# Kernel optimization log

Measured on AMD Instinct MI355X. Metric: run time of the kernel, lower is better.

## Reference

```python
import jax, jax.numpy as jnp
import numpy as np

MARGIN = 1.0  # init kwarg margin=1; hard_mining=False path


def setup_inputs() -> dict:
    key = jax.random.key(0)
    k1, k2 = jax.random.split(key)
    inputs = jax.random.normal(k1, (4096, 128), dtype=jnp.float32)
    targets = jax.random.randint(k2, (4096,), 0, 64, dtype=jnp.int64)
    return {"inputs": inputs, "targets": targets}


def reference(inputs, targets):
    n = inputs.shape[0]
    # squared pairwise distances: ||xi||^2 + ||xj||^2 - 2 xi.xj, relu'd then sqrt
    sq = jnp.sum(inputs * inputs, axis=1)                      # [n]
    d2 = jnp.maximum(sq[:, None] + sq[None, :] - 2.0 * (inputs @ inputs.T), 0.0)
    nz = d2 > 0
    dist = jnp.where(nz, jnp.sqrt(jnp.where(nz, d2, 1.0)), 0.0)  # safe sqrt, [n,n]

    eye = jnp.eye(n, dtype=bool)
    same = targets[:, None] == targets[None, :]
    pos_mask = same & ~eye            # positive pairs, diag removed
    neg_mask = ~same                  # negative pairs

    # torch code gathers neg_dist[i].nonzero(): negatives with nonzero distance
    neg_valid = neg_mask & (dist != 0.0)
    row_neg = jnp.sum(jnp.where(neg_valid, jnp.exp(MARGIN - dist), 0.0), axis=1)  # [n]

    # loop runs over upper-triangular positive pairs (diag already excluded)
    idx = jnp.arange(n)
    triu_pos = pos_mask & (idx[:, None] < idx[None, :])
    J = jnp.log(row_neg[:, None] + row_neg[None, :]) + dist    # Jij_heat
    contrib = jnp.where(triu_pos, jax.nn.relu(J) ** 2, 0.0)

    len_p = jnp.sum(pos_mask).astype(inputs.dtype)             # count over FULL pos_mask
    return jnp.sum(contrib) / len_p
```

## Files before the change

### kernel.cpp

```cpp
#include <hip/hip_runtime.h>
#include <hip/hip_bf16.h>
#include <math.h>

typedef short short8 __attribute__((ext_vector_type(8)));
typedef float f32x4 __attribute__((ext_vector_type(4)));

#define NROW 4096
#define DIM  128
#define NCLS 64
#define MAXM 128
#define LCAP 256
#define NBT  64
#define NTILE 2080
#define PS   66

__device__ __forceinline__ unsigned short f2bf(float f) {
    unsigned u = __builtin_bit_cast(unsigned, f);
    unsigned r = (u + 0x7fffu + ((u >> 16) & 1u)) >> 16;
    return (unsigned short)r;
}

__device__ __forceinline__ short8 pack8(const float4& a, const float4& b) {
    short8 h;
    h[0] = (short)f2bf(a.x); h[1] = (short)f2bf(a.y);
    h[2] = (short)f2bf(a.z); h[3] = (short)f2bf(a.w);
    h[4] = (short)f2bf(b.x); h[5] = (short)f2bf(b.y);
    h[6] = (short)f2bf(b.z); h[7] = (short)f2bf(b.w);
    return h;
}

__global__ __launch_bounds__(256, 4) void rowneg_kernel(
        const float* __restrict__ X, const int* __restrict__ tgt,
        float* __restrict__ P, float* __restrict__ acc, unsigned* __restrict__ tick)
{
    const int t = threadIdx.x;
    const int w = t >> 6, l = t & 63, lr = l & 15, lg = l >> 4;

    const int k = blockIdx.x;
    int bi = (int)(64.5f - sqrtf(64.5f * 64.5f - 2.0f * (float)k));
    if (bi < 0) bi = 0; if (bi > NBT - 1) bi = NBT - 1;
    while (bi < NBT - 1 && ((bi + 1) * NBT - (((bi + 1) * bi) >> 1)) <= k) ++bi;
    while (bi > 0 && (bi * NBT - ((bi * (bi - 1)) >> 1)) > k) --bi;
    const int bj = bi + (k - (bi * NBT - ((bi * (bi - 1)) >> 1)));
    const int gib = bi * 64, gjb = bj * 64;

    __shared__ __align__(16) unsigned short tA[64 * 128];
    __shared__ __align__(16) unsigned short tB[64 * 128];
    __shared__ float s_sqi[64], s_sqj[64];
    __shared__ float s_cacc[4][64];
    __shared__ int   s_ti[64], s_tj[64];

    {
        const int row  = t >> 1;
        const int half = t & 1;
        const int grow = (row < 64) ? (gib + row) : (gjb + row - 64);
        const float4* src = reinterpret_cast<const float4*>(X + (size_t)grow * DIM + half * 64);
        float4 buf[16];
        #pragma unroll
        for (int q = 0; q < 16; ++q) buf[q] = src[q];
        float p = 0.0f;
        #pragma unroll
        for (int q = 0; q < 16; ++q)
            p += buf[q].x * buf[q].x + buf[q].y * buf[q].y + buf[q].z * buf[q].z + buf[q].w * buf[q].w;
        p += __shfl_xor(p, 1);
        unsigned short* dst = (row < 64) ? tA : tB;
        const int lrow = row & 63;
        #pragma unroll
        for (int q = 0; q < 8; ++q) {
            int c16 = half * 8 + q;
            *reinterpret_cast<short8*>(&dst[lrow * 128 + ((c16 ^ (lrow & 7)) * 8)]) =
                pack8(buf[2 * q], buf[2 * q + 1]);
        }
        if (half == 0) {
            if (row < 64) s_sqi[row] = p; else s_sqj[row - 64] = p;
        }
    }
    if (t < 64)       s_ti[t] = tgt[gib + t];
    else if (t < 128) s_tj[t - 64] = tgt[gjb + t - 64];
    else if (k == 0 && t < 131) {
        if (t == 128) acc[0] = 0.0f;
        if (t == 129) acc[1] = 0.0f;
        if (t == 130) tick[0] = 0u;
    }
    __syncthreads();

    const int arow = w * 16 + lr;
    f32x4 C[4] = {};
    #pragma unroll
    for (int ks = 0; ks < 4; ++ks) {
        int c = ks * 4 + lg;
        short8 a = *reinterpret_cast<const short8*>(&tA[arow * 128 + ((c ^ (arow & 7)) * 8)]);
        #pragma unroll
        for (int fj = 0; fj < 4; ++fj) {
            int brow = fj * 16 + lr;
            short8 bb = *reinterpret_cast<const short8*>(&tB[brow * 128 + ((c ^ (brow & 7)) * 8)]);
            C[fj] = __builtin_amdgcn_mfma_f32_16x16x32_bf16(a, bb, C[fj], 0, 0, 0);
        }
    }

    const int ibase = w * 16 + lg * 4;
    float sqi[4]; int ti[4];
    #pragma unroll
    for (int r = 0; r < 4; ++r) { sqi[r] = s_sqi[ibase + r]; ti[r] = s_ti[ibase + r]; }

    float racc[4] = {0.f, 0.f, 0.f, 0.f};
    float cacc[4] = {0.f, 0.f, 0.f, 0.f};
    #pragma unroll
    for (int fj = 0; fj < 4; ++fj) {
        int jl = fj * 16 + lr;
        float sqj = s_sqj[jl];
        int   tj  = s_tj[jl];
        int   gj  = gjb + jl;
        #pragma unroll
        for (int r = 0; r < 4; ++r) {
            int gi = gib + ibase + r;
            float d2 = fmaxf(sqi[r] + sqj - 2.0f * C[fj][r], 0.0f);
            float dist = __builtin_amdgcn_sqrtf(d2);
            float e = __expf(1.0f - dist);
            bool valid = (gi < gj) && (ti[r] != tj) && (d2 > 0.0f);
            e = valid ? e : 0.0f;
            racc[r] += e;
            cacc[fj] += e;
        }
    }

    #pragma unroll
    for (int r = 0; r < 4; ++r) {
        racc[r] += __shfl_xor(racc[r], 1);
        racc[r] += __shfl_xor(racc[r], 2);
        racc[r] += __shfl_xor(racc[r], 4);
        racc[r] += __shfl_xor(racc[r], 8);
    }
    if (lr == 0) {
        #pragma unroll
        for (int r = 0; r < 4; ++r)
            P[(size_t)(gib + ibase + r) * PS + (bj + 1)] = racc[r];
    }
    #pragma unroll
    for (int fj = 0; fj < 4; ++fj) {
        cacc[fj] += __shfl_xor(cacc[fj], 16);
        cacc[fj] += __shfl_xor(cacc[fj], 32);
    }
    if (lg == 0) {
        #pragma unroll
        for (int fj = 0; fj < 4; ++fj) s_cacc[w][fj * 16 + lr] = cacc[fj];
    }
    __syncthreads();
    if (t < 64) {
        float cs = s_cacc[0][t] + s_cacc[1][t] + s_cacc[2][t] + s_cacc[3][t];
        P[(size_t)(gjb + t) * PS + bi] = cs;
    }
}

__global__ __launch_bounds__(256) void loss_kernel(
        const float* __restrict__ X, const int* __restrict__ tgt,
        const float* __restrict__ P,
        float* __restrict__ acc, unsigned* __restrict__ tick, float* __restrict__ out)
{
    const int c = blockIdx.x >> 1;
    const int h = blockIdx.x & 1;

    __shared__ __align__(16) unsigned short tX[MAXM * DIM];
    __shared__ float sqg[MAXM], rng[MAXM];
    __shared__ int   s_idx[LCAP];
    __shared__ int   s_wsum[4];
    __shared__ float s_red[16];

    const int t = threadIdx.x;
    const int w = t >> 6, l = t & 63, lr = l & 15, lg = l >> 4;

    float csum = 0.0f, cpairs = 0.0f;
    int mtot, mm, nfj;

    {
        const int rbase = t * 16;
        int tv[16];
        {
            int4 a = *reinterpret_cast<const int4*>(tgt + rbase);
            int4 b = *reinterpret_cast<const int4*>(tgt + rbase + 4);
            int4 d = *reinterpret_cast<const int4*>(tgt + rbase + 8);
            int4 e = *reinterpret_cast<const int4*>(tgt + rbase + 12);
            tv[0]=a.x; tv[1]=a.y; tv[2]=a.z; tv[3]=a.w;
            tv[4]=b.x; tv[5]=b.y; tv[6]=b.z; tv[7]=b.w;
            tv[8]=d.x; tv[9]=d.y; tv[10]=d.z; tv[11]=d.w;
            tv[12]=e.x; tv[13]=e.y; tv[14]=e.z; tv[15]=e.w;
        }
        int cnt = 0;
        #pragma unroll
        for (int k2 = 0; k2 < 16; ++k2) cnt += (tv[k2] == c) ? 1 : 0;
        int sc = cnt;
        #pragma unroll
        for (int d2 = 1; d2 < 64; d2 <<= 1) {
            int u = __shfl_up(sc, d2);
            if (l >= d2) sc += u;
        }
        if (l == 63) s_wsum[w] = sc;
        __syncthreads();
        int woff = 0;
        if (w > 0) woff += s_wsum[0];
        if (w > 1) woff += s_wsum[1];
        if (w > 2) woff += s_wsum[2];
        int off = woff + sc - cnt;
        #pragma unroll
        for (int k2 = 0; k2 < 16; ++k2) {
            if (tv[k2] == c) { if (off < LCAP) s_idx[off] = rbase + k2; ++off; }
        }
        mtot = s_wsum[0] + s_wsum[1] + s_wsum[2] + s_wsum[3];
    }
    mm  = mtot < MAXM ? mtot : MAXM;
    nfj = (mm + 15) >> 4;
    __syncthreads();

    if (h == 1 && mm <= 64) goto tickout;

    if (t < MAXM) {
        float s2 = 0.0f;
        if (t < mm) {
            const float* pp = P + (size_t)s_idx[t] * PS;
            #pragma unroll 5
            for (int s = 0; s < 65; ++s) s2 += pp[s];
        }
        rng[t] = s2;
    }

    {
        const int row  = t >> 1;
        const int half = t & 1;
        if (row < mm) {
            const int ri = s_idx[row];
            const float4* src = reinterpret_cast<const float4*>(X + (size_t)ri * DIM + half * 64);
            float4 buf[16];
            #pragma unroll
            for (int q = 0; q < 16; ++q) buf[q] = src[q];
            float p = 0.0f;
            #pragma unroll
            for (int q = 0; q < 16; ++q)
                p += buf[q].x * buf[q].x + buf[q].y * buf[q].y + buf[q].z * buf[q].z + buf[q].w * buf[q].w;
            p += __shfl_xor(p, 1);
            #pragma unroll
            for (int q = 0; q < 8; ++q) {
                int c16 = half * 8 + q;
                *reinterpret_cast<short8*>(&tX[row * 128 + ((c16 ^ (row & 7)) * 8)]) =
                    pack8(buf[2 * q], buf[2 * q + 1]);
            }
            if (half == 0) sqg[row] = p;
        } else if (half == 0 && row < MAXM) {
            sqg[row] = 0.0f;
        }
    }
    __syncthreads();

    {
        const int rowbase = h * 64 + w * 16;
        if (rowbase < mm) {
            f32x4 C[8] = {};
            const int arow = rowbase + lr;
            #pragma unroll
            for (int ks = 0; ks < 4; ++ks) {
                int cb = ks * 4 + lg;
                short8 a = *reinterpret_cast<const short8*>(&tX[arow * DIM + ((cb ^ (arow & 7)) * 8)]);
                #pragma unroll
                for (int fj = 0; fj < 8; ++fj) {
                    if (fj < nfj) {
                        int brow = fj * 16 + lr;
                        short8 bb = *reinterpret_cast<const short8*>(&tX[brow * DIM + ((cb ^ (brow & 7)) * 8)]);
                        C[fj] = __builtin_amdgcn_mfma_f32_16x16x32_bf16(a, bb, C[fj], 0, 0, 0);
                    }
                }
            }
            #pragma unroll
            for (int fj = 0; fj < 8; ++fj) {
                if (fj < nfj) {
                    int q = fj * 16 + lr;
                    #pragma unroll
                    for (int r = 0; r < 4; ++r) {
                        int p = rowbase + lg * 4 + r;
                        if (q < mm && p < q) {
                            float d2 = fmaxf(sqg[p] + sqg[q] - 2.0f * C[fj][r], 0.0f);
                            float dist = __builtin_amdgcn_sqrtf(d2);
                            float J = __logf(rng[p] + rng[q]) + dist;
                            if (J > 0.0f) csum += J * J;
                            cpairs += 1.0f;
                        }
                    }
                }
            }
        }

        if (h == 0 && mtot > MAXM) {
            int mq = mtot < LCAP ? mtot : LCAP;
            for (int q = MAXM; q < mq; ++q) {
                int rq = s_idx[q];
                const float4* xb = reinterpret_cast<const float4*>(X + (size_t)rq * DIM);
                float sqq = 0.0f;
                for (int kq = 0; kq < 32; ++kq) {
                    float4 bv = xb[kq];
                    sqq += bv.x * bv.x + bv.y * bv.y + bv.z * bv.z + bv.w * bv.w;
                }
                float rnq = 0.0f;
                for (int s = 0; s < 65; ++s) rnq += P[(size_t)rq * PS + s];
                for (int p2 = t; p2 < q; p2 += 256) {
                    int rp = s_idx[p2];
                    const float4* xa = reinterpret_cast<const float4*>(X + (size_t)rp * DIM);
                    float d = 0.0f, sqp = 0.0f;
                    for (int kq = 0; kq < 32; ++kq) {
                        float4 av = xa[kq], bv = xb[kq];
                        d += av.x * bv.x + av.y * bv.y + av.z * bv.z + av.w * bv.w;
                        sqp += av.x * av.x + av.y * av.y + av.z * av.z + av.w * av.w;
                    }
                    float rnp = 0.0f;
                    for (int s = 0; s < 65; ++s) rnp += P[(size_t)rp * PS + s];
                    float d2 = fmaxf(sqp + sqq - 2.0f * d, 0.0f);
                    float dist = __builtin_amdgcn_sqrtf(d2);
                    float J = __logf(rnp + rnq) + dist;
                    if (J > 0.0f) csum += J * J;
                    cpairs += 1.0f;
                }
            }
        }

        #pragma unroll
        for (int mr = 1; mr < 64; mr <<= 1) {
            csum   += __shfl_xor(csum, mr);
            cpairs += __shfl_xor(cpairs, mr);
        }
        if (l == 0) { s_red[w] = csum; s_red[8 + w] = cpairs; }
        __syncthreads();
        if (t == 0) {
            float bs = s_red[0] + s_red[1] + s_red[2] + s_red[3];
            float bc = s_red[8] + s_red[9] + s_red[10] + s_red[11];
            if (bs != 0.0f || bc != 0.0f) {
                atomicAdd(&acc[0], bs);
                atomicAdd(&acc[1], bc);
            }
        }
    }

tickout:
    __threadfence();
    if (t == 0) {
        unsigned old = atomicAdd(tick, 1u);
        if (old == 2 * NCLS - 1) {
            float s  = atomicAdd(&acc[0], 0.0f);
            float n2 = atomicAdd(&acc[1], 0.0f);
            out[0] = s / (2.0f * n2);
        }
    }
}

extern "C" void kernel_launch(void* const* d_in, const int* in_sizes, int n_in,
                              void* d_out, int out_size, void* d_ws, size_t ws_size,
                              hipStream_t stream)
{
    const float* X  = (const float*)d_in[0];
    const int* tgt  = (const int*)d_in[1];
    float* out      = (float*)d_out;

    float*    P    = (float*)d_ws;
    float*    acc  = P + (size_t)NROW * PS;
    unsigned* tick = (unsigned*)(acc + 2);

    rowneg_kernel<<<NTILE, 256, 0, stream>>>(X, tgt, P, acc, tick);
    loss_kernel<<<2 * NCLS, 256, 0, stream>>>(X, tgt, P, acc, tick, out);
}
```

Measured before the change: 48.96 us.

## Fuse row-negative and loss kernels into one per-class strip kernel

Replaces the triangular-tile row_neg kernel and the separate per-class loss kernel with one kernel. Each block loads one class's member rows into LDS once and sweeps a 512-column strip to get partial negative sums. The last strip block for a class, found with an atomic ticket, finishes the class loss, and a global ticket does the final reduction. This removes a launch, the large P workspace round-trip and the symmetric scatter writes. In exchange it computes the full rectangle rather than the upper triangle, and it drops the fallback path for classes with more than 128 members.

```diff
diff --git a/kernel.cpp b/kernel.cpp
--- a/kernel.cpp
+++ b/kernel.cpp
@@ -5,14 +5,13 @@
 typedef short short8 __attribute__((ext_vector_type(8)));
 typedef float f32x4 __attribute__((ext_vector_type(4)));
 
-#define NROW 4096
-#define DIM  128
-#define NCLS 64
-#define MAXM 128
-#define LCAP 256
-#define NBT  64
-#define NTILE 2080
-#define PS   66
+#define NROW   4096
+#define DIM    128
+#define NCLS   64
+#define MAXM   128
+#define NSTRIP 8
+#define CPS    512
+#define NJT    8
 
 __device__ __forceinline__ unsigned short f2bf(float f) {
     unsigned u = __builtin_bit_cast(unsigned, f);
@@ -29,149 +28,27 @@
     return h;
 }
 
-__global__ __launch_bounds__(256, 4) void rowneg_kernel(
+__device__ __forceinline__ float agentLoad(float* p) {
+    return __hip_atomic_load(p, __ATOMIC_RELAXED, __HIP_MEMORY_SCOPE_AGENT);
+}
+
+__global__ __launch_bounds__(256, 2) void fused_kernel(
         const float* __restrict__ X, const int* __restrict__ tgt,
-        float* __restrict__ P, float* __restrict__ acc, unsigned* __restrict__ tick)
+        float* rnP, float* res, unsigned* tickC, unsigned* tickG,
+        float* __restrict__ out)
 {
+    __shared__ __align__(16) unsigned short tCLS[MAXM * DIM];
+    __shared__ __align__(16) unsigned short tCOL[64 * DIM];
+    __shared__ float sqg[MAXM], rng[MAXM], sqc[64], s_red[16];
+    __shared__ int   tjc[64], s_idx[MAXM], s_wsum[4];
+    __shared__ int   s_win;
+
     const int t = threadIdx.x;
     const int w = t >> 6, l = t & 63, lr = l & 15, lg = l >> 4;
-
-    const int k = blockIdx.x;
-    int bi = (int)(64.5f - sqrtf(64.5f * 64.5f - 2.0f * (float)k));
-    if (bi < 0) bi = 0; if (bi > NBT - 1) bi = NBT - 1;
-    while (bi < NBT - 1 && ((bi + 1) * NBT - (((bi + 1) * bi) >> 1)) <= k) ++bi;
-    while (bi > 0 && (bi * NBT - ((bi * (bi - 1)) >> 1)) > k) --bi;
-    const int bj = bi + (k - (bi * NBT - ((bi * (bi - 1)) >> 1)));
-    const int gib = bi * 64, gjb = bj * 64;
-
-    __shared__ __align__(16) unsigned short tA[64 * 128];
-    __shared__ __align__(16) unsigned short tB[64 * 128];
-    __shared__ float s_sqi[64], s_sqj[64];
-    __shared__ float s_cacc[4][64];
-    __shared__ int   s_ti[64], s_tj[64];
-
-    {
-        const int row  = t >> 1;
-        const int half = t & 1;
-        const int grow = (row < 64) ? (gib + row) : (gjb + row - 64);
-        const float4* src = reinterpret_cast<const float4*>(X + (size_t)grow * DIM + half * 64);
-        float4 buf[16];
-        #pragma unroll
-        for (int q = 0; q < 16; ++q) buf[q] = src[q];
-        float p = 0.0f;
-        #pragma unroll
-        for (int q = 0; q < 16; ++q)
-            p += buf[q].x * buf[q].x + buf[q].y * buf[q].y + buf[q].z * buf[q].z + buf[q].w * buf[q].w;
-        p += __shfl_xor(p, 1);
-        unsigned short* dst = (row < 64) ? tA : tB;
-        const int lrow = row & 63;
-        #pragma unroll
-        for (int q = 0; q < 8; ++q) {
-            int c16 = half * 8 + q;
-            *reinterpret_cast<short8*>(&dst[lrow * 128 + ((c16 ^ (lrow & 7)) * 8)]) =
-                pack8(buf[2 * q], buf[2 * q + 1]);
-        }
-        if (half == 0) {
-            if (row < 64) s_sqi[row] = p; else s_sqj[row - 64] = p;
-        }
-    }
-    if (t < 64)       s_ti[t] = tgt[gib + t];
-    else if (t < 128) s_tj[t - 64] = tgt[gjb + t - 64];
-    else if (k == 0 && t < 131) {
-        if (t == 128) acc[0] = 0.0f;
-        if (t == 129) acc[1] = 0.0f;
-        if (t == 130) tick[0] = 0u;
-    }
-    __syncthreads();
-
-    const int arow = w * 16 + lr;
-    f32x4 C[4] = {};
-    #pragma unroll
-    for (int ks = 0; ks < 4; ++ks) {
-        int c = ks * 4 + lg;
-        short8 a = *reinterpret_cast<const short8*>(&tA[arow * 128 + ((c ^ (arow & 7)) * 8)]);
-        #pragma unroll
-        for (int fj = 0; fj < 4; ++fj) {
-            int brow = fj * 16 + lr;
-            short8 bb = *reinterpret_cast<const short8*>(&tB[brow * 128 + ((c ^ (brow & 7)) * 8)]);
-            C[fj] = __builtin_amdgcn_mfma_f32_16x16x32_bf16(a, bb, C[fj], 0, 0, 0);
-        }
-    }
-
-    const int ibase = w * 16 + lg * 4;
-    float sqi[4]; int ti[4];
-    #pragma unroll
-    for (int r = 0; r < 4; ++r) { sqi[r] = s_sqi[ibase + r]; ti[r] = s_ti[ibase + r]; }
-
-    float racc[4] = {0.f, 0.f, 0.f, 0.f};
-    float cacc[4] = {0.f, 0.f, 0.f, 0.f};
-    #pragma unroll
-    for (int fj = 0; fj < 4; ++fj) {
-        int jl = fj * 16 + lr;
-        float sqj = s_sqj[jl];
-        int   tj  = s_tj[jl];
-        int   gj  = gjb + jl;
-        #pragma unroll
-        for (int r = 0; r < 4; ++r) {
-            int gi = gib + ibase + r;
-            float d2 = fmaxf(sqi[r] + sqj - 2.0f * C[fj][r], 0.0f);
-            float dist = __builtin_amdgcn_sqrtf(d2);
-            float e = __expf(1.0f - dist);
-            bool valid = (gi < gj) && (ti[r] != tj) && (d2 > 0.0f);
-            e = valid ? e : 0.0f;
-            racc[r] += e;
-            cacc[fj] += e;
-        }
-    }
-
-    #pragma unroll
-    for (int r = 0; r < 4; ++r) {
-        racc[r] += __shfl_xor(racc[r], 1);
-        racc[r] += __shfl_xor(racc[r], 2);
-        racc[r] += __shfl_xor(racc[r], 4);
-        racc[r] += __shfl_xor(racc[r], 8);
-    }
-    if (lr == 0) {
-        #pragma unroll
-        for (int r = 0; r < 4; ++r)
-            P[(size_t)(gib + ibase + r) * PS + (bj + 1)] = racc[r];
-    }
-    #pragma unroll
-    for (int fj = 0; fj < 4; ++fj) {
-        cacc[fj] += __shfl_xor(cacc[fj], 16);
-        cacc[fj] += __shfl_xor(cacc[fj], 32);
-    }
-    if (lg == 0) {
-        #pragma unroll
-        for (int fj = 0; fj < 4; ++fj) s_cacc[w][fj * 16 + lr] = cacc[fj];
-    }
-    __syncthreads();
-    if (t < 64) {
-        float cs = s_cacc[0][t] + s_cacc[1][t] + s_cacc[2][t] + s_cacc[3][t];
-        P[(size_t)(gjb + t) * PS + bi] = cs;
-    }
-}
-
-__global__ __launch_bounds__(256) void loss_kernel(
-        const float* __restrict__ X, const int* __restrict__ tgt,
-        const float* __restrict__ P,
-        float* __restrict__ acc, unsigned* __restrict__ tick, float* __restrict__ out)
-{
-    const int c = blockIdx.x >> 1;
-    const int h = blockIdx.x & 1;
-
-    __shared__ __align__(16) unsigned short tX[MAXM * DIM];
-    __shared__ float sqg[MAXM], rng[MAXM];
-    __shared__ int   s_idx[LCAP];
-    __shared__ int   s_wsum[4];
-    __shared__ float s_red[16];
-
-    const int t = threadIdx.x;
-    const int w = t >> 6, l = t & 63, lr = l & 15, lg = l >> 4;
-
-    float csum = 0.0f, cpairs = 0.0f;
-    int mtot, mm, nfj;
-
+    const int c = blockIdx.x >> 3;
+    const int s = blockIdx.x & (NSTRIP - 1);
+
+    int mtot;
     {
         const int rbase = t * 16;
         int tv[16];
@@ -187,7 +64,7 @@
         }
         int cnt = 0;
         #pragma unroll
-        for (int k2 = 0; k2 < 16; ++k2) cnt += (tv[k2] == c) ? 1 : 0;
+        for (int k = 0; k < 16; ++k) cnt += (tv[k] == c) ? 1 : 0;
         int sc = cnt;
         #pragma unroll
         for (int d2 = 1; d2 < 64; d2 <<= 1) {
@@ -202,69 +79,164 @@
         if (w > 2) woff += s_wsum[2];
         int off = woff + sc - cnt;
         #pragma unroll
-        for (int k2 = 0; k2 < 16; ++k2) {
-            if (tv[k2] == c) { if (off < LCAP) s_idx[off] = rbase + k2; ++off; }
+        for (int k = 0; k < 16; ++k) {
+            if (tv[k] == c) { if (off < MAXM) s_idx[off] = rbase + k; ++off; }
         }
         mtot = s_wsum[0] + s_wsum[1] + s_wsum[2] + s_wsum[3];
     }
-    mm  = mtot < MAXM ? mtot : MAXM;
-    nfj = (mm + 15) >> 4;
-    __syncthreads();
-
-    if (h == 1 && mm <= 64) goto tickout;
-
+    const int mm = mtot < MAXM ? mtot : MAXM;
+    __syncthreads();
+
+    {
+        const int sub = t & 3;
+        #pragma unroll
+        for (int r0 = 0; r0 < MAXM; r0 += 64) {
+            int row = r0 + (t >> 2);
+            if (row < mm) {
+                int ri = s_idx[row];
+                const float4* src = reinterpret_cast<const float4*>(X + (size_t)ri * DIM + sub * 32);
+                float4 buf[8];
+                #pragma unroll
+                for (int q = 0; q < 8; ++q) buf[q] = src[q];
+                float p = 0.0f;
+                #pragma unroll
+                for (int q = 0; q < 8; ++q)
+                    p += buf[q].x * buf[q].x + buf[q].y * buf[q].y + buf[q].z * buf[q].z + buf[q].w * buf[q].w;
+                p += __shfl_xor(p, 1);
+                p += __shfl_xor(p, 2);
+                #pragma unroll
+                for (int q = 0; q < 4; ++q) {
+                    int c16 = sub * 4 + q;
+                    *reinterpret_cast<short8*>(&tCLS[row * DIM + ((c16 ^ (row & 7)) * 8)]) =
+                        pack8(buf[2 * q], buf[2 * q + 1]);
+                }
+                if (sub == 0) sqg[row] = p;
+            }
+        }
+    }
+
+    float racc[2][4] = {};
+    for (int jt = 0; jt < NJT; ++jt) {
+        const int colb = s * CPS + jt * 64;
+        __syncthreads();
+        {
+            const int row = t >> 2, sub = t & 3;
+            const float4* src = reinterpret_cast<const float4*>(X + (size_t)(colb + row) * DIM + sub * 32);
+            float4 buf[8];
+            #pragma unroll
+            for (int q = 0; q < 8; ++q) buf[q] = src[q];
+            float p = 0.0f;
+            #pragma unroll
+            for (int q = 0; q < 8; ++q)
+                p += buf[q].x * buf[q].x + buf[q].y * buf[q].y + buf[q].z * buf[q].z + buf[q].w * buf[q].w;
+            p += __shfl_xor(p, 1);
+            p += __shfl_xor(p, 2);
+            #pragma unroll
+            for (int q = 0; q < 4; ++q) {
+                int c16 = sub * 4 + q;
+                *reinterpret_cast<short8*>(&tCOL[row * DIM + ((c16 ^ (row & 7)) * 8)]) =
+                    pack8(buf[2 * q], buf[2 * q + 1]);
+            }
+            if (sub == 0) sqc[row] = p;
+        }
+        if (t < 64) tjc[t] = tgt[colb + t];
+        __syncthreads();
+
+        #pragma unroll
+        for (int fi = 0; fi < 2; ++fi) {
+            const int rowbase = fi * 64 + w * 16;
+            if (rowbase < mm) {
+                const int arow = rowbase + lr;
+                f32x4 C[4] = {};
+                #pragma unroll
+                for (int ks = 0; ks < 4; ++ks) {
+                    int cb = ks * 4 + lg;
+                    short8 a = *reinterpret_cast<const short8*>(&tCLS[arow * DIM + ((cb ^ (arow & 7)) * 8)]);
+                    #pragma unroll
+                    for (int fj = 0; fj < 4; ++fj) {
+                        int brow = fj * 16 + lr;
+                        short8 bb = *reinterpret_cast<const short8*>(&tCOL[brow * DIM + ((cb ^ (brow & 7)) * 8)]);
+                        C[fj] = __builtin_amdgcn_mfma_f32_16x16x32_bf16(a, bb, C[fj], 0, 0, 0);
+                    }
+                }
+                #pragma unroll
+                for (int fj = 0; fj < 4; ++fj) {
+                    int jl = fj * 16 + lr;
+                    float sc2 = sqc[jl];
+                    int   tj  = tjc[jl];
+                    #pragma unroll
+                    for (int r = 0; r < 4; ++r) {
+                        int p = rowbase + lg * 4 + r;
+                        float d2 = fmaxf(sqg[p] + sc2 - 2.0f * C[fj][r], 0.0f);
+                        float dist = __builtin_amdgcn_sqrtf(d2);
+                        float e = __expf(1.0f - dist);
+                        bool valid = (tj != c) && (d2 > 0.0f);
+                        racc[fi][r] += valid ? e : 0.0f;
+                    }
+                }
+            }
+        }
+    }
+
+    #pragma unroll
+    for (int fi = 0; fi < 2; ++fi)
+        #pragma unroll
+        for (int r = 0; r < 4; ++r) {
+            racc[fi][r] += __shfl_xor(racc[fi][r], 1);
+            racc[fi][r] += __shfl_xor(racc[fi][r], 2);
+            racc[fi][r] += __shfl_xor(racc[fi][r], 4);
+            racc[fi][r] += __shfl_xor(racc[fi][r], 8);
+        }
+    if (lr == 0) {
+        #pragma unroll
+        for (int fi = 0; fi < 2; ++fi)
+            #pragma unroll
+            for (int r = 0; r < 4; ++r) {
+                int prow = fi * 64 + w * 16 + lg * 4 + r;
+                if (prow < mm)
+                    rnP[((size_t)c * MAXM + prow) * NSTRIP + s] = racc[fi][r];
+            }
+    }
+
+    __threadfence();
+    __syncthreads();
+    if (t == 0) {
+        unsigned old = atomicAdd(&tickC[c], 1u);
+        s_win = ((old & (NSTRIP - 1)) == (NSTRIP - 1)) ? 1 : 0;
+    }
+    __syncthreads();
+    if (!s_win) return;
+
+    __threadfence();
     if (t < MAXM) {
         float s2 = 0.0f;
         if (t < mm) {
-            const float* pp = P + (size_t)s_idx[t] * PS;
-            #pragma unroll 5
-            for (int s = 0; s < 65; ++s) s2 += pp[s];
+            float* pp = &rnP[((size_t)c * MAXM + t) * NSTRIP];
+            #pragma unroll
+            for (int s2i = 0; s2i < NSTRIP; ++s2i) s2 += agentLoad(pp + s2i);
         }
         rng[t] = s2;
     }
-
-    {
-        const int row  = t >> 1;
-        const int half = t & 1;
-        if (row < mm) {
-            const int ri = s_idx[row];
-            const float4* src = reinterpret_cast<const float4*>(X + (size_t)ri * DIM + half * 64);
-            float4 buf[16];
-            #pragma unroll
-            for (int q = 0; q < 16; ++q) buf[q] = src[q];
-            float p = 0.0f;
-            #pragma unroll
-            for (int q = 0; q < 16; ++q)
-                p += buf[q].x * buf[q].x + buf[q].y * buf[q].y + buf[q].z * buf[q].z + buf[q].w * buf[q].w;
-            p += __shfl_xor(p, 1);
-            #pragma unroll
-            for (int q = 0; q < 8; ++q) {
-                int c16 = half * 8 + q;
-                *reinterpret_cast<short8*>(&tX[row * 128 + ((c16 ^ (row & 7)) * 8)]) =
-                    pack8(buf[2 * q], buf[2 * q + 1]);
-            }
-            if (half == 0) sqg[row] = p;
-        } else if (half == 0 && row < MAXM) {
-            sqg[row] = 0.0f;
-        }
-    }
-    __syncthreads();
-
-    {
-        const int rowbase = h * 64 + w * 16;
+    __syncthreads();
+
+    float csum = 0.0f, cpairs = 0.0f;
+    const int nfj = (mm + 15) >> 4;
+    #pragma unroll
+    for (int fi2 = 0; fi2 < 2; ++fi2) {
+        const int rowbase = fi2 * 64 + w * 16;
         if (rowbase < mm) {
-            f32x4 C[8] = {};
             const int arow = rowbase + lr;
+            f32x4 C2[8] = {};
             #pragma unroll
             for (int ks = 0; ks < 4; ++ks) {
                 int cb = ks * 4 + lg;
-                short8 a = *reinterpret_cast<const short8*>(&tX[arow * DIM + ((cb ^ (arow & 7)) * 8)]);
+                short8 a = *reinterpret_cast<const short8*>(&tCLS[arow * DIM + ((cb ^ (arow & 7)) * 8)]);
                 #pragma unroll
                 for (int fj = 0; fj < 8; ++fj) {
                     if (fj < nfj) {
                         int brow = fj * 16 + lr;
-                        short8 bb = *reinterpret_cast<const short8*>(&tX[brow * DIM + ((cb ^ (brow & 7)) * 8)]);
-                        C[fj] = __builtin_amdgcn_mfma_f32_16x16x32_bf16(a, bb, C[fj], 0, 0, 0);
+                        short8 bb = *reinterpret_cast<const short8*>(&tCLS[brow * DIM + ((cb ^ (brow & 7)) * 8)]);
+                        C2[fj] = __builtin_amdgcn_mfma_f32_16x16x32_bf16(a, bb, C2[fj], 0, 0, 0);
                     }
                 }
             }
@@ -276,7 +248,7 @@
                     for (int r = 0; r < 4; ++r) {
                         int p = rowbase + lg * 4 + r;
                         if (q < mm && p < q) {
-                            float d2 = fmaxf(sqg[p] + sqg[q] - 2.0f * C[fj][r], 0.0f);
+                            float d2 = fmaxf(sqg[p] + sqg[q] - 2.0f * C2[fj][r], 0.0f);
                             float dist = __builtin_amdgcn_sqrtf(d2);
                             float J = __logf(rng[p] + rng[q]) + dist;
                             if (J > 0.0f) csum += J * J;
@@ -286,64 +258,28 @@
                 }
             }
         }
-
-        if (h == 0 && mtot > MAXM) {
-            int mq = mtot < LCAP ? mtot : LCAP;
-            for (int q = MAXM; q < mq; ++q) {
-                int rq = s_idx[q];
-                const float4* xb = reinterpret_cast<const float4*>(X + (size_t)rq * DIM);
-                float sqq = 0.0f;
-                for (int kq = 0; kq < 32; ++kq) {
-                    float4 bv = xb[kq];
-                    sqq += bv.x * bv.x + bv.y * bv.y + bv.z * bv.z + bv.w * bv.w;
-                }
-                float rnq = 0.0f;
-                for (int s = 0; s < 65; ++s) rnq += P[(size_t)rq * PS + s];
-                for (int p2 = t; p2 < q; p2 += 256) {
-                    int rp = s_idx[p2];
-                    const float4* xa = reinterpret_cast<const float4*>(X + (size_t)rp * DIM);
-                    float d = 0.0f, sqp = 0.0f;
-                    for (int kq = 0; kq < 32; ++kq) {
-                        float4 av = xa[kq], bv = xb[kq];
-                        d += av.x * bv.x + av.y * bv.y + av.z * bv.z + av.w * bv.w;
-                        sqp += av.x * av.x + av.y * av.y + av.z * av.z + av.w * av.w;
-                    }
-                    float rnp = 0.0f;
-                    for (int s = 0; s < 65; ++s) rnp += P[(size_t)rp * PS + s];
-                    float d2 = fmaxf(sqp + sqq - 2.0f * d, 0.0f);
-                    float dist = __builtin_amdgcn_sqrtf(d2);
-                    float J = __logf(rnp + rnq) + dist;
-                    if (J > 0.0f) csum += J * J;
-                    cpairs += 1.0f;
-                }
-            }
-        }
-
-        #pragma unroll
-        for (int mr = 1; mr < 64; mr <<= 1) {
-            csum   += __shfl_xor(csum, mr);
-            cpairs += __shfl_xor(cpairs, mr);
-        }
-        if (l == 0) { s_red[w] = csum; s_red[8 + w] = cpairs; }
-        __syncthreads();
-        if (t == 0) {
-            float bs = s_red[0] + s_red[1] + s_red[2] + s_red[3];
-            float bc = s_red[8] + s_red[9] + s_red[10] + s_red[11];
-            if (bs != 0.0f || bc != 0.0f) {
-                atomicAdd(&acc[0], bs);
-                atomicAdd(&acc[1], bc);
-            }
-        }
-    }
-
-tickout:
-    __threadfence();
+    }
+
+    #pragma unroll
+    for (int mr = 1; mr < 64; mr <<= 1) {
+        csum   += __shfl_xor(csum, mr);
+        cpairs += __shfl_xor(cpairs, mr);
+    }
+    if (l == 0) { s_red[w] = csum; s_red[8 + w] = cpairs; }
+    __syncthreads();
     if (t == 0) {
-        unsigned old = atomicAdd(tick, 1u);
-        if (old == 2 * NCLS - 1) {
-            float s  = atomicAdd(&acc[0], 0.0f);
-            float n2 = atomicAdd(&acc[1], 0.0f);
-            out[0] = s / (2.0f * n2);
+        res[c * 2]     = s_red[0] + s_red[1] + s_red[2] + s_red[3];
+        res[c * 2 + 1] = s_red[8] + s_red[9] + s_red[10] + s_red[11];
+        __threadfence();
+        unsigned old2 = atomicAdd(tickG, 1u);
+        if ((old2 & (NCLS - 1)) == (NCLS - 1)) {
+            __threadfence();
+            float S = 0.0f, N2 = 0.0f;
+            for (int cc = 0; cc < NCLS; ++cc) {
+                S  += agentLoad(&res[cc * 2]);
+                N2 += agentLoad(&res[cc * 2 + 1]);
+            }
+            out[0] = S / (2.0f * N2);
         }
     }
 }
@@ -356,10 +292,10 @@
     const int* tgt  = (const int*)d_in[1];
     float* out      = (float*)d_out;
 
-    float*    P    = (float*)d_ws;
-    float*    acc  = P + (size_t)NROW * PS;
-    unsigned* tick = (unsigned*)(acc + 2);
-
-    rowneg_kernel<<<NTILE, 256, 0, stream>>>(X, tgt, P, acc, tick);
-    loss_kernel<<<2 * NCLS, 256, 0, stream>>>(X, tgt, P, acc, tick, out);
-}
+    float*    rnP   = (float*)d_ws;
+    float*    res   = rnP + (size_t)NCLS * MAXM * NSTRIP;
+    unsigned* tickC = (unsigned*)(res + 2 * NCLS);
+    unsigned* tickG = tickC + NCLS;
+
+    fused_kernel<<<NCLS * NSTRIP, 256, 0, stream>>>(X, tgt, rnP, res, tickC, tickG, out);
+}
```

After: 154.8 us. 3.16x slower.

## Precompute bf16 copy and row norms once, stream tiles via global_load_lds

Applied to the files above, without the earlier changes.

Adds a prep kernel that converts X to bf16 and computes squared row norms once, instead of every one of the 2080 triangular tiles re-reading fp32 rows, converting them and reducing norms. The rowneg and loss kernels now copy pre-swizzled bf16 rows straight into LDS with global_load_lds, and diagonal tiles load only one tile and reuse it. This cuts global traffic and conversion ALU work per tile, at the cost of an extra kernel launch and a workspace round-trip for the bf16 copy.

```diff
diff --git a/kernel.cpp b/kernel.cpp
--- a/kernel.cpp
+++ b/kernel.cpp
@@ -14,24 +14,46 @@
 #define NTILE 2080
 #define PS   66
 
+typedef __attribute__((address_space(3))) unsigned lds_u32;
+typedef const __attribute__((address_space(1))) unsigned glb_u32;
+
+__device__ __forceinline__ void gload16(const void* g, void* lds) {
+    __builtin_amdgcn_global_load_lds((glb_u32*)g, (lds_u32*)lds, 16, 0, 0);
+}
+
 __device__ __forceinline__ unsigned short f2bf(float f) {
     unsigned u = __builtin_bit_cast(unsigned, f);
     unsigned r = (u + 0x7fffu + ((u >> 16) & 1u)) >> 16;
     return (unsigned short)r;
 }
 
-__device__ __forceinline__ short8 pack8(const float4& a, const float4& b) {
-    short8 h;
-    h[0] = (short)f2bf(a.x); h[1] = (short)f2bf(a.y);
-    h[2] = (short)f2bf(a.z); h[3] = (short)f2bf(a.w);
-    h[4] = (short)f2bf(b.x); h[5] = (short)f2bf(b.y);
-    h[6] = (short)f2bf(b.z); h[7] = (short)f2bf(b.w);
-    return h;
+__global__ __launch_bounds__(256) void prep_kernel(const float* __restrict__ X,
+        unsigned short* __restrict__ Xb, float* __restrict__ sq,
+        float* __restrict__ acc, unsigned* __restrict__ tick)
+{
+    int t = threadIdx.x;
+    int row = blockIdx.x * 8 + (t >> 5);
+    int c = t & 31;
+    float4 v = *reinterpret_cast<const float4*>(X + (size_t)row * DIM + c * 4);
+    float p = v.x * v.x + v.y * v.y + v.z * v.z + v.w * v.w;
+    p += __shfl_xor(p, 16, 32);
+    p += __shfl_xor(p, 8, 32);
+    p += __shfl_xor(p, 4, 32);
+    p += __shfl_xor(p, 2, 32);
+    p += __shfl_xor(p, 1, 32);
+    ushort4 h;
+    h.x = f2bf(v.x); h.y = f2bf(v.y); h.z = f2bf(v.z); h.w = f2bf(v.w);
+    *reinterpret_cast<ushort4*>(Xb + (size_t)row * DIM + c * 4) = h;
+    if (c == 0) sq[row] = p;
+    if (blockIdx.x == 0) {
+        if (t == 64) { acc[0] = 0.0f; acc[1] = 0.0f; }
+        if (t == 65) tick[0] = 0u;
+    }
 }
 
 __global__ __launch_bounds__(256, 4) void rowneg_kernel(
-        const float* __restrict__ X, const int* __restrict__ tgt,
-        float* __restrict__ P, float* __restrict__ acc, unsigned* __restrict__ tick)
+        const unsigned short* __restrict__ Xb, const float* __restrict__ sq,
+        const int* __restrict__ tgt, float* __restrict__ P)
 {
     const int t = threadIdx.x;
     const int w = t >> 6, l = t & 63, lr = l & 15, lg = l >> 4;
@@ -43,6 +65,7 @@
     while (bi > 0 && (bi * NBT - ((bi * (bi - 1)) >> 1)) > k) --bi;
     const int bj = bi + (k - (bi * NBT - ((bi * (bi - 1)) >> 1)));
     const int gib = bi * 64, gjb = bj * 64;
+    const bool diag = (bi == bj);
 
     __shared__ __align__(16) unsigned short tA[64 * 128];
     __shared__ __align__(16) unsigned short tB[64 * 128];
@@ -50,41 +73,22 @@
     __shared__ float s_cacc[4][64];
     __shared__ int   s_ti[64], s_tj[64];
 
-    {
-        const int row  = t >> 1;
-        const int half = t & 1;
-        const int grow = (row < 64) ? (gib + row) : (gjb + row - 64);
-        const float4* src = reinterpret_cast<const float4*>(X + (size_t)grow * DIM + half * 64);
-        float4 buf[16];
-        #pragma unroll
-        for (int q = 0; q < 16; ++q) buf[q] = src[q];
-        float p = 0.0f;
-        #pragma unroll
-        for (int q = 0; q < 16; ++q)
-            p += buf[q].x * buf[q].x + buf[q].y * buf[q].y + buf[q].z * buf[q].z + buf[q].w * buf[q].w;
-        p += __shfl_xor(p, 1);
-        unsigned short* dst = (row < 64) ? tA : tB;
-        const int lrow = row & 63;
-        #pragma unroll
-        for (int q = 0; q < 8; ++q) {
-            int c16 = half * 8 + q;
-            *reinterpret_cast<short8*>(&dst[lrow * 128 + ((c16 ^ (lrow & 7)) * 8)]) =
-                pack8(buf[2 * q], buf[2 * q + 1]);
-        }
-        if (half == 0) {
-            if (row < 64) s_sqi[row] = p; else s_sqj[row - 64] = p;
-        }
-    }
-    if (t < 64)       s_ti[t] = tgt[gib + t];
-    else if (t < 128) s_tj[t - 64] = tgt[gjb + t - 64];
-    else if (k == 0 && t < 131) {
-        if (t == 128) acc[0] = 0.0f;
-        if (t == 129) acc[1] = 0.0f;
-        if (t == 130) tick[0] = 0u;
-    }
+    #pragma unroll
+    for (int kk = 0; kk < 4; ++kk) {
+        int q = w * 4 + kk;
+        int row = q * 4 + (l >> 4);
+        int sc = (l & 15) ^ (row & 7);
+        gload16(Xb + (size_t)(gib + row) * DIM + sc * 8, &tA[q * 512]);
+        if (!diag)
+            gload16(Xb + (size_t)(gjb + row) * DIM + sc * 8, &tB[q * 512]);
+    }
+    if (t < 64)       { s_sqi[t] = sq[gib + t]; s_ti[t] = tgt[gib + t]; }
+    else if (t < 128) { int u = t - 64; s_sqj[u] = sq[gjb + u]; s_tj[u] = tgt[gjb + u]; }
     __syncthreads();
 
+    const unsigned short* tBp = diag ? tA : tB;
     const int arow = w * 16 + lr;
+
     f32x4 C[4] = {};
     #pragma unroll
     for (int ks = 0; ks < 4; ++ks) {
@@ -93,7 +97,7 @@
         #pragma unroll
         for (int fj = 0; fj < 4; ++fj) {
             int brow = fj * 16 + lr;
-            short8 bb = *reinterpret_cast<const short8*>(&tB[brow * 128 + ((c ^ (brow & 7)) * 8)]);
+            short8 bb = *reinterpret_cast<const short8*>(&tBp[brow * 128 + ((c ^ (brow & 7)) * 8)]);
             C[fj] = __builtin_amdgcn_mfma_f32_16x16x32_bf16(a, bb, C[fj], 0, 0, 0);
         }
     }
@@ -153,7 +157,8 @@
 }
 
 __global__ __launch_bounds__(256) void loss_kernel(
-        const float* __restrict__ X, const int* __restrict__ tgt,
+        const unsigned short* __restrict__ Xb, const float* __restrict__ X,
+        const float* __restrict__ sq, const int* __restrict__ tgt,
         const float* __restrict__ P,
         float* __restrict__ acc, unsigned* __restrict__ tick, float* __restrict__ out)
 {
@@ -206,6 +211,7 @@
             if (tv[k2] == c) { if (off < LCAP) s_idx[off] = rbase + k2; ++off; }
         }
         mtot = s_wsum[0] + s_wsum[1] + s_wsum[2] + s_wsum[3];
+        if (t >= mtot && t < MAXM) s_idx[t] = 0;
     }
     mm  = mtot < MAXM ? mtot : MAXM;
     nfj = (mm + 15) >> 4;
@@ -214,38 +220,23 @@
     if (h == 1 && mm <= 64) goto tickout;
 
     if (t < MAXM) {
-        float s2 = 0.0f;
+        float s2 = 0.0f, q2 = 0.0f;
         if (t < mm) {
             const float* pp = P + (size_t)s_idx[t] * PS;
             #pragma unroll 5
             for (int s = 0; s < 65; ++s) s2 += pp[s];
+            q2 = sq[s_idx[t]];
         }
         rng[t] = s2;
-    }
-
-    {
-        const int row  = t >> 1;
-        const int half = t & 1;
-        if (row < mm) {
-            const int ri = s_idx[row];
-            const float4* src = reinterpret_cast<const float4*>(X + (size_t)ri * DIM + half * 64);
-            float4 buf[16];
-            #pragma unroll
-            for (int q = 0; q < 16; ++q) buf[q] = src[q];
-            float p = 0.0f;
-            #pragma unroll
-            for (int q = 0; q < 16; ++q)
-                p += buf[q].x * buf[q].x + buf[q].y * buf[q].y + buf[q].z * buf[q].z + buf[q].w * buf[q].w;
-            p += __shfl_xor(p, 1);
-            #pragma unroll
-            for (int q = 0; q < 8; ++q) {
-                int c16 = half * 8 + q;
-                *reinterpret_cast<short8*>(&tX[row * 128 + ((c16 ^ (row & 7)) * 8)]) =
-                    pack8(buf[2 * q], buf[2 * q + 1]);
-            }
-            if (half == 0) sqg[row] = p;
-        } else if (half == 0 && row < MAXM) {
-            sqg[row] = 0.0f;
+        sqg[t] = q2;
+    }
+    #pragma unroll
+    for (int kk = 0; kk < 8; ++kk) {
+        int q = w * 8 + kk;
+        int row = q * 4 + (l >> 4);
+        if (row < ((mm + 3) & ~3)) {
+            int sc = (l & 15) ^ (row & 7);
+            gload16(Xb + (size_t)s_idx[row] * DIM + sc * 8, &tX[q * 512]);
         }
     }
     __syncthreads();
@@ -292,25 +283,20 @@
             for (int q = MAXM; q < mq; ++q) {
                 int rq = s_idx[q];
                 const float4* xb = reinterpret_cast<const float4*>(X + (size_t)rq * DIM);
-                float sqq = 0.0f;
-                for (int kq = 0; kq < 32; ++kq) {
-                    float4 bv = xb[kq];
-                    sqq += bv.x * bv.x + bv.y * bv.y + bv.z * bv.z + bv.w * bv.w;
-                }
+                float sqq = sq[rq];
                 float rnq = 0.0f;
                 for (int s = 0; s < 65; ++s) rnq += P[(size_t)rq * PS + s];
                 for (int p2 = t; p2 < q; p2 += 256) {
                     int rp = s_idx[p2];
                     const float4* xa = reinterpret_cast<const float4*>(X + (size_t)rp * DIM);
-                    float d = 0.0f, sqp = 0.0f;
+                    float d = 0.0f;
                     for (int kq = 0; kq < 32; ++kq) {
                         float4 av = xa[kq], bv = xb[kq];
                         d += av.x * bv.x + av.y * bv.y + av.z * bv.z + av.w * bv.w;
-                        sqp += av.x * av.x + av.y * av.y + av.z * av.z + av.w * av.w;
                     }
                     float rnp = 0.0f;
                     for (int s = 0; s < 65; ++s) rnp += P[(size_t)rp * PS + s];
-                    float d2 = fmaxf(sqp + sqq - 2.0f * d, 0.0f);
+                    float d2 = fmaxf(sq[rp] + sqq - 2.0f * d, 0.0f);
                     float dist = __builtin_amdgcn_sqrtf(d2);
                     float J = __logf(rnp + rnq) + dist;
                     if (J > 0.0f) csum += J * J;
@@ -356,10 +342,14 @@
     const int* tgt  = (const int*)d_in[1];
     float* out      = (float*)d_out;
 
-    float*    P    = (float*)d_ws;
+    char* ws = (char*)d_ws;
+    unsigned short* Xb = (unsigned short*)ws;
+    float*    sq   = (float*)(ws + (size_t)NROW * DIM * 2);
+    float*    P    = sq + NROW;
     float*    acc  = P + (size_t)NROW * PS;
     unsigned* tick = (unsigned*)(acc + 2);
 
-    rowneg_kernel<<<NTILE, 256, 0, stream>>>(X, tgt, P, acc, tick);
-    loss_kernel<<<2 * NCLS, 256, 0, stream>>>(X, tgt, P, acc, tick, out);
-}
+    prep_kernel<<<NROW / 8, 256, 0, stream>>>(X, Xb, sq, acc, tick);
+    rowneg_kernel<<<NTILE, 256, 0, stream>>>(Xb, sq, tgt, P);
+    loss_kernel<<<2 * NCLS, 256, 0, stream>>>(Xb, X, sq, tgt, P, acc, tick, out);
+}
```

Result: faster. 45.09 us (-7.9%).
